# Kernel tuning notes

Measured on AMD Instinct MI355X. Metric: run time of the kernel, lower is better.

## Reference

```python
import jax, jax.numpy as jnp
import numpy as np

N_EMBD = 1024
N_HEAD = 16
HEAD_DIM = N_EMBD // N_HEAD
SCALE = 1.0 / np.sqrt(HEAD_DIM).astype(np.float32)


def setup_inputs() -> dict:
    key = jax.random.key(0)
    ks = jax.random.split(key, 9)
    B, T = 2, 2048
    std = 1.0 / np.sqrt(N_EMBD).astype(np.float32)
    x = jax.random.normal(ks[0], (B, T, N_EMBD), dtype=jnp.float32)
    Wq = jax.random.normal(ks[1], (N_EMBD, N_EMBD), dtype=jnp.float32) * std
    Wk = jax.random.normal(ks[2], (N_EMBD, N_EMBD), dtype=jnp.float32) * std
    Wv = jax.random.normal(ks[3], (N_EMBD, N_EMBD), dtype=jnp.float32) * std
    Wo = jax.random.normal(ks[4], (N_EMBD, N_EMBD), dtype=jnp.float32) * std
    bq = jax.random.normal(ks[5], (N_EMBD,), dtype=jnp.float32) * 0.01
    bk = jax.random.normal(ks[6], (N_EMBD,), dtype=jnp.float32) * 0.01
    bv = jax.random.normal(ks[7], (N_EMBD,), dtype=jnp.float32) * 0.01
    bo = jax.random.normal(ks[8], (N_EMBD,), dtype=jnp.float32) * 0.01
    return {"x": x, "Wq": Wq, "bq": bq, "Wk": Wk, "bk": bk,
            "Wv": Wv, "bv": bv, "Wo": Wo, "bo": bo}


def reference(x, Wq, bq, Wk, bk, Wv, bv, Wo, bo):
    B, T, C = x.shape
    # project and split heads: (B, H, T, D)
    def heads(y):
        return y.reshape(B, T, N_HEAD, HEAD_DIM).transpose(0, 2, 1, 3)
    q = heads(x @ Wq.T + bq)
    k = heads(x @ Wk.T + bk)
    v = heads(x @ Wv.T + bv)
    # materialized causal attention (matches the torch module's math)
    att = jnp.einsum("bhqd,bhkd->bhqk", q, k) * SCALE
    causal = jnp.tril(jnp.ones((T, T), dtype=bool))
    att = jnp.where(causal, att, -jnp.inf)
    att = jax.nn.softmax(att, axis=-1)
    out = jnp.einsum("bhqk,bhkd->bhqd", att, v)
    out = out.transpose(0, 2, 1, 3).reshape(B, T, C)
    return out @ Wo.T + bo
```

## Files before the change

kernel.cpp:

```cpp
#include <hip/hip_runtime.h>
#include <stdint.h>

typedef unsigned short u16;
typedef __attribute__((ext_vector_type(8))) short short8;
typedef __attribute__((ext_vector_type(4))) float f32x4;
typedef __attribute__((ext_vector_type(16))) float f32x16;

__device__ __forceinline__ u16 f2bf(float f) {
  union { float f; unsigned int u; } c; c.f = f;
  return (u16)((c.u + 0x7FFFu + ((c.u >> 16) & 1u)) >> 16);
}

__device__ __forceinline__ float bf2f(u16 v) {
  union { unsigned int u; float f; } c; c.u = ((unsigned int)v) << 16;
  return c.f;
}

__device__ __forceinline__ f32x4 mfma16(short8 a, short8 b, f32x4 c) {
  return __builtin_amdgcn_mfma_f32_16x16x32_bf16(a, b, c, 0, 0, 0);
}

__device__ __forceinline__ f32x16 mfma32(short8 a, short8 b, f32x16 c) {
  return __builtin_amdgcn_mfma_f32_32x32x16_bf16(a, b, c, 0, 0, 0);
}

__device__ __forceinline__ void gl_lds16(const u16* g, u16* l) {
  __builtin_amdgcn_global_load_lds((const __attribute__((address_space(1))) void*)g,
                                   (__attribute__((address_space(3))) void*)l, 16, 0, 0);
}

__global__ __launch_bounds__(256) void cast_all(
    const float* __restrict__ x, const float* __restrict__ wq, const float* __restrict__ wk,
    const float* __restrict__ wv, const float* __restrict__ wo,
    u16* __restrict__ xb, u16* __restrict__ wqb, u16* __restrict__ wkb,
    u16* __restrict__ wvb, u16* __restrict__ wob) {
  int b = blockIdx.x;
  const float* src; u16* dst; int i;
  if (b < 4096)      { src = x;  dst = xb;  i = b * 256 + threadIdx.x; }
  else if (b < 5120) { src = wq; dst = wqb; i = (b - 4096) * 256 + threadIdx.x; }
  else if (b < 6144) { src = wk; dst = wkb; i = (b - 5120) * 256 + threadIdx.x; }
  else if (b < 7168) { src = wv; dst = wvb; i = (b - 6144) * 256 + threadIdx.x; }
  else               { src = wo; dst = wob; i = (b - 7168) * 256 + threadIdx.x; }
  float4 v = ((const float4*)src)[i];
  ushort4 o;
  o.x = f2bf(v.x); o.y = f2bf(v.y); o.z = f2bf(v.z); o.w = f2bf(v.w);
  ((ushort4*)dst)[i] = o;
}

__global__ __launch_bounds__(256) void qkv_gemm(
    const u16* __restrict__ xb, const u16* __restrict__ wqb, const u16* __restrict__ wkb,
    const u16* __restrict__ wvb, const float* __restrict__ bq, const float* __restrict__ bk,
    const float* __restrict__ bv, u16* __restrict__ Qb, u16* __restrict__ Kb,
    u16* __restrict__ VTb) {
  __shared__ __align__(16) u16 As[2][128 * 64];
  __shared__ __align__(16) u16 Bs[2][128 * 64];
  const int id = blockIdx.x;
  const int s = id >> 3;
  const int mblk = (id & 7) + ((s & 3) << 3);
  const int z = (s >> 2) % 3;
  const int nblk = s / 12;
  const u16* __restrict__ W = (z == 0) ? wqb : (z == 1) ? wkb : wvb;
  const float* __restrict__ bias = (z == 0) ? bq : (z == 1) ? bk : bv;
  const int m0 = mblk * 128, n0 = nblk * 128;
  const int tid = threadIdx.x, lane = tid & 63, wave = tid >> 6;
  const int wr = (wave >> 1) * 64, wc = (wave & 1) * 64;
  const int fr = lane & 15, fg = lane >> 4;
  const int lrow = lane >> 3;
  const int lcol = (((lane & 7) ^ (lrow & 7)) * 8);

  const u16* ga = xb + (size_t)(m0 + wave * 32 + lrow) * 1024 + lcol;
  const u16* gb = W  + (size_t)(n0 + wave * 32 + lrow) * 1024 + lcol;

  auto stage = [&](int k0, int b) {
    u16* la = As[b] + wave * 2048;
    u16* lb = Bs[b] + wave * 2048;
#pragma unroll
    for (int i = 0; i < 4; ++i) {
      gl_lds16(ga + k0 + (size_t)(8 * i) * 1024, la + i * 512);
      gl_lds16(gb + k0 + (size_t)(8 * i) * 1024, lb + i * 512);
    }
  };

  f32x4 acc[4][4] = {};

  stage(0, 0);
  asm volatile("s_waitcnt vmcnt(0)" ::: "memory");
  __builtin_amdgcn_s_barrier();
  __builtin_amdgcn_sched_barrier(0);

  for (int t = 0; t < 16; ++t) {
    const int cur = t & 1;
    if (t < 15) stage((t + 1) * 64, cur ^ 1);
    __builtin_amdgcn_sched_barrier(0);
    const u16* Ac = As[cur];
    const u16* Bc = Bs[cur];
#pragma unroll
    for (int kk = 0; kk < 2; ++kk) {
      short8 a[4], b[4];
#pragma unroll
      for (int i = 0; i < 4; ++i)
        a[i] = *(const short8*)(Ac + (wr + i * 16 + fr) * 64 +
                                (((kk * 4 + fg) ^ (fr & 7)) * 8));
#pragma unroll
      for (int i = 0; i < 4; ++i)
        b[i] = *(const short8*)(Bc + (wc + i * 16 + fr) * 64 +
                                (((kk * 4 + fg) ^ (fr & 7)) * 8));
      __builtin_amdgcn_s_setprio(1);
#pragma unroll
      for (int i = 0; i < 4; ++i)
#pragma unroll
        for (int j = 0; j < 4; ++j) acc[i][j] = mfma16(a[i], b[j], acc[i][j]);
      __builtin_amdgcn_s_setprio(0);
    }
    asm volatile("s_waitcnt vmcnt(0)" ::: "memory");
    __builtin_amdgcn_s_barrier();
    __builtin_amdgcn_sched_barrier(0);
  }

  const float qsc = (z == 0) ? (0.125f * 1.44269504088896f) : 1.0f;
#pragma unroll
  for (int j = 0; j < 4; ++j) {
    const int col = n0 + wc + j * 16 + fr;
    const float bcol = bias[col];
    const int h = col >> 6, d = col & 63;
#pragma unroll
    for (int i = 0; i < 4; ++i) {
#pragma unroll
      for (int r = 0; r < 4; ++r) {
        const int m = m0 + wr + i * 16 + fg * 4 + r;
        const int bi = m >> 11, t = m & 2047;
        const u16 o = f2bf((acc[i][j][r] + bcol) * qsc);
        const size_t bse = (size_t)(bi * 16 + h) << 17;
        if (z == 0)      Qb[bse + (size_t)t * 64 + d] = o;
        else if (z == 1) Kb[bse + (size_t)t * 64 + d] = o;
        else             VTb[bse + (size_t)d * 2048 + t] = o;
      }
    }
  }
}

__global__ __launch_bounds__(256, 2) void attn_kernel(
    const u16* __restrict__ Qb, const u16* __restrict__ Kb, const u16* __restrict__ VTb,
    u16* __restrict__ aOb) {
  __shared__ __align__(16) char smem[49152];
  __shared__ float Mll[4][2][64];
  u16* Ow = (u16*)smem;
  const int id = blockIdx.x;
  const int xcd = id & 7, wbl = id >> 3;
  const int cu = wbl & 31, rr = wbl >> 5;
  const int g = cu >> 2;
  const int bh = xcd + ((cu & 3) << 3);
  const int j = (rr == 0) ? 31 - g : (rr == 1) ? 16 + g : (rr == 2) ? 15 - g : g;
  const int tid = threadIdx.x, lane = tid & 63, wave = tid >> 6;
  const int l31 = lane & 31, hi = lane >> 5;
  const size_t base = (size_t)bh << 17;
  const int bi = bh >> 4, h = bh & 15;
  const int q0 = j * 64;

  u16* kb0 = (u16*)(smem + wave * 12288);
  u16* kb1 = (u16*)(smem + wave * 12288 + 4096);
  u16* vb  = (u16*)(smem + wave * 12288 + 8192);

  short8 qf[2][4];
  {
    const u16* qp = Qb + base + (size_t)(q0 + l31) * 64 + hi * 8;
#pragma unroll
    for (int mi = 0; mi < 2; ++mi)
#pragma unroll
      for (int st = 0; st < 4; ++st)
        qf[mi][st] = *(const short8*)(qp + mi * 32 * 64 + st * 16);
  }

  f32x16 oacc[2][2] = {};
  float lrun[2] = {0.f, 0.f};

  auto stageK = [&](int t0, u16* kb) {
    const u16* kp = Kb + base + (size_t)(t0 + (lane >> 3)) * 64 +
                    (((lane & 7) ^ ((lane >> 3) & 7)) * 8);
#pragma unroll
    for (int i = 0; i < 4; ++i) gl_lds16(kp + (size_t)(8 * i) * 64, kb + i * 512);
  };
  auto stageV = [&](int t0) {
    const u16* vp = VTb + base + (size_t)(lane >> 2) * 2048 + t0 +
                    (((lane & 3) ^ ((lane >> 2) & 3)) * 8);
#pragma unroll
    for (int i = 0; i < 4; ++i) gl_lds16(vp + (size_t)(16 * i) * 2048, vb + i * 512);
  };

  const int tmax = 2 * j + 1;
  if (wave <= tmax) {
    int buf = 0;
    stageK(wave * 32, kb0);
    stageV(wave * 32);
    for (int tu = wave; tu <= tmax; tu += 4) {
      const int t0 = tu * 32;
      const bool more = (tu + 4 <= tmax);
      if (more) {
        stageK((tu + 4) * 32, buf ? kb0 : kb1);
        asm volatile("s_waitcnt vmcnt(4)" ::: "memory");
      } else {
        asm volatile("s_waitcnt vmcnt(0)" ::: "memory");
      }
      __builtin_amdgcn_sched_barrier(0);
      const char* kb = (const char*)(buf ? kb1 : kb0);

      short8 kf[4];
#pragma unroll
      for (int st = 0; st < 4; ++st)
        kf[st] = *(const short8*)(kb + l31 * 128 + (((st * 2 + hi) ^ (l31 & 7)) << 4));
      short8 vf[2][2];
#pragma unroll
      for (int nb = 0; nb < 2; ++nb)
#pragma unroll
        for (int ks = 0; ks < 2; ++ks)
          vf[nb][ks] = *(const short8*)((const char*)vb + (nb * 32 + l31) * 64 +
                                        (((ks * 2 + hi) ^ (l31 & 3)) << 4));

#pragma unroll
      for (int mi = 0; mi < 2; ++mi) {
        f32x16 s = {};
        __builtin_amdgcn_s_setprio(1);
        s = mfma32(kf[0], qf[mi][0], s);
        s = mfma32(kf[1], qf[mi][1], s);
        s = mfma32(kf[2], qf[mi][2], s);
        s = mfma32(kf[3], qf[mi][3], s);
        __builtin_amdgcn_s_setprio(0);

        if (t0 + 31 > q0 + mi * 32) {
          const int qv = q0 + mi * 32 + l31;
#pragma unroll
          for (int r = 0; r < 16; ++r) {
            const int tl = t0 + (r & 3) + ((r >> 2) << 3) + hi * 4;
            if (tl > qv) s[r] = -1e30f;
          }
        }

        float rs = 0.f;
#pragma unroll
        for (int r = 0; r < 16; ++r) {
          const float pv = exp2f(s[r]);
          s[r] = pv;
          rs += pv;
        }
        lrun[mi] += rs;

        uint32_t w0, w1, w2, w3, w4, w5, w6, w7;
        asm("v_cvt_pk_bf16_f32 %0, %1, %2" : "=v"(w0) : "v"(s[0]),  "v"(s[1]));
        asm("v_cvt_pk_bf16_f32 %0, %1, %2" : "=v"(w1) : "v"(s[2]),  "v"(s[3]));
        asm("v_cvt_pk_bf16_f32 %0, %1, %2" : "=v"(w2) : "v"(s[4]),  "v"(s[5]));
        asm("v_cvt_pk_bf16_f32 %0, %1, %2" : "=v"(w3) : "v"(s[6]),  "v"(s[7]));
        asm("v_cvt_pk_bf16_f32 %0, %1, %2" : "=v"(w4) : "v"(s[8]),  "v"(s[9]));
        asm("v_cvt_pk_bf16_f32 %0, %1, %2" : "=v"(w5) : "v"(s[10]), "v"(s[11]));
        asm("v_cvt_pk_bf16_f32 %0, %1, %2" : "=v"(w6) : "v"(s[12]), "v"(s[13]));
        asm("v_cvt_pk_bf16_f32 %0, %1, %2" : "=v"(w7) : "v"(s[14]), "v"(s[15]));
        asm("v_permlane32_swap_b32 %0, %1" : "+v"(w0), "+v"(w2));
        asm("v_permlane32_swap_b32 %0, %1" : "+v"(w1), "+v"(w3));
        asm("v_permlane32_swap_b32 %0, %1" : "+v"(w4), "+v"(w6));
        asm("v_permlane32_swap_b32 %0, %1" : "+v"(w5), "+v"(w7));
        short8 pa0, pa1;
        {
          uint32_t* p0 = (uint32_t*)&pa0;
          p0[0] = w0; p0[1] = w1; p0[2] = w2; p0[3] = w3;
          uint32_t* p1 = (uint32_t*)&pa1;
          p1[0] = w4; p1[1] = w5; p1[2] = w6; p1[3] = w7;
        }

        __builtin_amdgcn_s_setprio(1);
        oacc[mi][0] = mfma32(pa0, vf[0][0], oacc[mi][0]);
        oacc[mi][0] = mfma32(pa1, vf[0][1], oacc[mi][0]);
        oacc[mi][1] = mfma32(pa0, vf[1][0], oacc[mi][1]);
        oacc[mi][1] = mfma32(pa1, vf[1][1], oacc[mi][1]);
        __builtin_amdgcn_s_setprio(0);
      }

      if (more) {
        asm volatile("s_waitcnt lgkmcnt(0)" ::: "memory");
        __builtin_amdgcn_sched_barrier(0);
        stageV((tu + 4) * 32);
      }
      buf ^= 1;
    }
  }

  __syncthreads();
#pragma unroll
  for (int mi = 0; mi < 2; ++mi) Mll[wave][hi][mi * 32 + l31] = lrun[mi];
#pragma unroll
  for (int mi = 0; mi < 2; ++mi)
#pragma unroll
    for (int nb = 0; nb < 2; ++nb)
#pragma unroll
      for (int r = 0; r < 16; ++r) {
        const int q = mi * 32 + (r & 3) + ((r >> 2) << 3) + hi * 4;
        Ow[(wave * 64 + q) * 72 + nb * 32 + l31] = f2bf(oacc[mi][nb][r]);
      }
  __syncthreads();

  const int rq = tid >> 2, c0 = (tid & 3) * 16;
  float lt = 0.f;
#pragma unroll
  for (int w = 0; w < 4; ++w)
#pragma unroll
    for (int gg = 0; gg < 2; ++gg) lt += Mll[w][gg][rq];
  const float inv = __builtin_amdgcn_rcpf(lt);
  float o[16] = {};
#pragma unroll
  for (int w = 0; w < 4; ++w) {
    const u16* orow = &Ow[(w * 64 + rq) * 72 + c0];
    short8 a = *(const short8*)orow;
    short8 b = *(const short8*)(orow + 8);
#pragma unroll
    for (int i = 0; i < 8; ++i) {
      o[i]     += bf2f((u16)a[i]);
      o[8 + i] += bf2f((u16)b[i]);
    }
  }
  short8 r0, r1;
#pragma unroll
  for (int i = 0; i < 8; ++i) {
    r0[i] = (short)f2bf(o[i] * inv);
    r1[i] = (short)f2bf(o[8 + i] * inv);
  }
  u16* op = aOb + ((size_t)bi * 2048 + q0 + rq) * 1024 + h * 64 + c0;
  *(short8*)op = r0;
  *(short8*)(op + 8) = r1;
}

__global__ __launch_bounds__(256) void out_gemm(
    const u16* __restrict__ Ab, const u16* __restrict__ Wb, const float* __restrict__ bo,
    float* __restrict__ out) {
  __shared__ __align__(16) u16 As[2][128 * 64];
  __shared__ __align__(16) u16 Bs[2][128 * 64];
  const int id = blockIdx.x;
  const int s = id >> 3;
  const int m0 = ((id & 7) + ((s & 3) << 3)) * 128;
  const int n0 = (s >> 2) * 128;
  const int tid = threadIdx.x, lane = tid & 63, wave = tid >> 6;
  const int wr = (wave >> 1) * 64, wc = (wave & 1) * 64;
  const int fr = lane & 15, fg = lane >> 4;
  const int lrow = lane >> 3;
  const int lcol = (((lane & 7) ^ (lrow & 7)) * 8);

  const u16* ga = Ab + (size_t)(m0 + wave * 32 + lrow) * 1024 + lcol;
  const u16* gb = Wb + (size_t)(n0 + wave * 32 + lrow) * 1024 + lcol;

  auto stage = [&](int k0, int b) {
    u16* la = As[b] + wave * 2048;
    u16* lb = Bs[b] + wave * 2048;
#pragma unroll
    for (int i = 0; i < 4; ++i) {
      gl_lds16(ga + k0 + (size_t)(8 * i) * 1024, la + i * 512);
      gl_lds16(gb + k0 + (size_t)(8 * i) * 1024, lb + i * 512);
    }
  };

  f32x4 acc[4][4] = {};

  stage(0, 0);
  asm volatile("s_waitcnt vmcnt(0)" ::: "memory");
  __builtin_amdgcn_s_barrier();
  __builtin_amdgcn_sched_barrier(0);

  for (int t = 0; t < 16; ++t) {
    const int cur = t & 1;
    if (t < 15) stage((t + 1) * 64, cur ^ 1);
    __builtin_amdgcn_sched_barrier(0);
    const u16* Ac = As[cur];
    const u16* Bc = Bs[cur];
#pragma unroll
    for (int kk = 0; kk < 2; ++kk) {
      short8 a[4], b[4];
#pragma unroll
      for (int i = 0; i < 4; ++i)
        a[i] = *(const short8*)(Ac + (wr + i * 16 + fr) * 64 +
                                (((kk * 4 + fg) ^ (fr & 7)) * 8));
#pragma unroll
      for (int i = 0; i < 4; ++i)
        b[i] = *(const short8*)(Bc + (wc + i * 16 + fr) * 64 +
                                (((kk * 4 + fg) ^ (fr & 7)) * 8));
      __builtin_amdgcn_s_setprio(1);
#pragma unroll
      for (int i = 0; i < 4; ++i)
#pragma unroll
        for (int j = 0; j < 4; ++j) acc[i][j] = mfma16(a[i], b[j], acc[i][j]);
      __builtin_amdgcn_s_setprio(0);
    }
    asm volatile("s_waitcnt vmcnt(0)" ::: "memory");
    __builtin_amdgcn_s_barrier();
    __builtin_amdgcn_sched_barrier(0);
  }

#pragma unroll
  for (int j = 0; j < 4; ++j) {
    const int col = n0 + wc + j * 16 + fr;
    const float bcol = bo[col];
#pragma unroll
    for (int i = 0; i < 4; ++i)
#pragma unroll
      for (int r = 0; r < 4; ++r) {
        const int m = m0 + wr + i * 16 + fg * 4 + r;
        out[(size_t)m * 1024 + col] = acc[i][j][r] + bcol;
      }
  }
}

extern "C" void kernel_launch(void* const* d_in, const int* in_sizes, int n_in,
                              void* d_out, int out_size, void* d_ws, size_t ws_size,
                              hipStream_t stream) {
  (void)in_sizes; (void)n_in; (void)out_size; (void)ws_size;
  const float* x  = (const float*)d_in[0];
  const float* Wq = (const float*)d_in[1];
  const float* bq = (const float*)d_in[2];
  const float* Wk = (const float*)d_in[3];
  const float* bk = (const float*)d_in[4];
  const float* Wv = (const float*)d_in[5];
  const float* bv = (const float*)d_in[6];
  const float* Wo = (const float*)d_in[7];
  const float* bo = (const float*)d_in[8];
  float* out = (float*)d_out;
  char* ws = (char*)d_ws;

  const size_t MB = 1024 * 1024;
  u16* xb  = (u16*)(ws);
  u16* wqb = (u16*)(ws + 8 * MB);
  u16* wkb = (u16*)(ws + 10 * MB);
  u16* wvb = (u16*)(ws + 12 * MB);
  u16* wob = (u16*)(ws + 14 * MB);
  u16* Qb  = (u16*)(ws + 16 * MB);
  u16* Kb  = (u16*)(ws + 24 * MB);
  u16* VTb = (u16*)(ws + 32 * MB);
  u16* aOb = (u16*)(ws + 40 * MB);

  cast_all<<<8192, 256, 0, stream>>>(x, Wq, Wk, Wv, Wo, xb, wqb, wkb, wvb, wob);
  qkv_gemm<<<768, 256, 0, stream>>>(xb, wqb, wkb, wvb, bq, bk, bv, Qb, Kb, VTb);
  attn_kernel<<<1024, 256, 0, stream>>>(Qb, Kb, VTb, aOb);
  out_gemm<<<256, 256, 0, stream>>>(aOb, wob, bo, out);
}
```

Measured before the change: 123.8 us.

## Give each wave private LDS tiles in QKV and output GEMMs, dropping block barriers

Each wave now loads only its own 64x32 slices of A and B into a private LDS region, so the per-iteration block-wide s_barrier and full vmcnt(0) waits are gone. The loop uses a K-step of 32 with a partial vmcnt wait, so the next stage's loads stay in flight while the current one is consumed. QKV block indexing is also changed so the projection index z is the outermost dimension. The cost is no sharing of A/B tiles between waves: each wave fetches its own copy, doubling global/L2 traffic per block. The loop also runs twice as many iterations, each with less work.

```diff
diff --git a/kernel.cpp b/kernel.cpp
--- a/kernel.cpp
+++ b/kernel.cpp
@@ -52,68 +52,67 @@
     const u16* __restrict__ wvb, const float* __restrict__ bq, const float* __restrict__ bk,
     const float* __restrict__ bv, u16* __restrict__ Qb, u16* __restrict__ Kb,
     u16* __restrict__ VTb) {
-  __shared__ __align__(16) u16 As[2][128 * 64];
-  __shared__ __align__(16) u16 Bs[2][128 * 64];
+  __shared__ __align__(16) char smem[65536];
   const int id = blockIdx.x;
-  const int s = id >> 3;
-  const int mblk = (id & 7) + ((s & 3) << 3);
-  const int z = (s >> 2) % 3;
-  const int nblk = s / 12;
+  const int z = id >> 8;
+  const int u = id & 255;
+  const int mblk = (u & 7) + (((u >> 3) & 3) << 3);
+  const int nblk = u >> 5;
   const u16* __restrict__ W = (z == 0) ? wqb : (z == 1) ? wkb : wvb;
   const float* __restrict__ bias = (z == 0) ? bq : (z == 1) ? bk : bv;
   const int m0 = mblk * 128, n0 = nblk * 128;
   const int tid = threadIdx.x, lane = tid & 63, wave = tid >> 6;
   const int wr = (wave >> 1) * 64, wc = (wave & 1) * 64;
   const int fr = lane & 15, fg = lane >> 4;
-  const int lrow = lane >> 3;
-  const int lcol = (((lane & 7) ^ (lrow & 7)) * 8);
-
-  const u16* ga = xb + (size_t)(m0 + wave * 32 + lrow) * 1024 + lcol;
-  const u16* gb = W  + (size_t)(n0 + wave * 32 + lrow) * 1024 + lcol;
+  const int r16 = lane >> 2;
+  const int cswz = (lane & 3) ^ (r16 & 3);
+
+  u16* la0 = (u16*)(smem + wave * 16384);
+  u16* la1 = (u16*)(smem + wave * 16384 + 4096);
+  u16* lb0 = (u16*)(smem + wave * 16384 + 8192);
+  u16* lb1 = (u16*)(smem + wave * 16384 + 12288);
+
+  const u16* gA = xb + (size_t)(m0 + wr + r16) * 1024 + cswz * 8;
+  const u16* gB = W  + (size_t)(n0 + wc + r16) * 1024 + cswz * 8;
 
   auto stage = [&](int k0, int b) {
-    u16* la = As[b] + wave * 2048;
-    u16* lb = Bs[b] + wave * 2048;
+    u16* la = b ? la1 : la0;
+    u16* lb = b ? lb1 : lb0;
 #pragma unroll
     for (int i = 0; i < 4; ++i) {
-      gl_lds16(ga + k0 + (size_t)(8 * i) * 1024, la + i * 512);
-      gl_lds16(gb + k0 + (size_t)(8 * i) * 1024, lb + i * 512);
+      gl_lds16(gA + k0 + (size_t)(i * 16) * 1024, la + i * 512);
+      gl_lds16(gB + k0 + (size_t)(i * 16) * 1024, lb + i * 512);
     }
   };
 
   f32x4 acc[4][4] = {};
-
   stage(0, 0);
-  asm volatile("s_waitcnt vmcnt(0)" ::: "memory");
-  __builtin_amdgcn_s_barrier();
-  __builtin_amdgcn_sched_barrier(0);
-
-  for (int t = 0; t < 16; ++t) {
+
+  for (int t = 0; t < 32; ++t) {
     const int cur = t & 1;
-    if (t < 15) stage((t + 1) * 64, cur ^ 1);
+    if (t < 31) {
+      stage((t + 1) * 32, cur ^ 1);
+      asm volatile("s_waitcnt vmcnt(8)" ::: "memory");
+    } else {
+      asm volatile("s_waitcnt vmcnt(0)" ::: "memory");
+    }
     __builtin_amdgcn_sched_barrier(0);
-    const u16* Ac = As[cur];
-    const u16* Bc = Bs[cur];
-#pragma unroll
-    for (int kk = 0; kk < 2; ++kk) {
-      short8 a[4], b[4];
-#pragma unroll
-      for (int i = 0; i < 4; ++i)
-        a[i] = *(const short8*)(Ac + (wr + i * 16 + fr) * 64 +
-                                (((kk * 4 + fg) ^ (fr & 7)) * 8));
-#pragma unroll
-      for (int i = 0; i < 4; ++i)
-        b[i] = *(const short8*)(Bc + (wc + i * 16 + fr) * 64 +
-                                (((kk * 4 + fg) ^ (fr & 7)) * 8));
-      __builtin_amdgcn_s_setprio(1);
-#pragma unroll
-      for (int i = 0; i < 4; ++i)
-#pragma unroll
-        for (int j = 0; j < 4; ++j) acc[i][j] = mfma16(a[i], b[j], acc[i][j]);
-      __builtin_amdgcn_s_setprio(0);
-    }
-    asm volatile("s_waitcnt vmcnt(0)" ::: "memory");
-    __builtin_amdgcn_s_barrier();
+    const u16* Ac = cur ? la1 : la0;
+    const u16* Bc = cur ? lb1 : lb0;
+    short8 a[4], b[4];
+#pragma unroll
+    for (int i = 0; i < 4; ++i)
+      a[i] = *(const short8*)(Ac + (i * 16 + fr) * 32 + ((fg ^ (fr & 3)) * 8));
+#pragma unroll
+    for (int i = 0; i < 4; ++i)
+      b[i] = *(const short8*)(Bc + (i * 16 + fr) * 32 + ((fg ^ (fr & 3)) * 8));
+    __builtin_amdgcn_s_setprio(1);
+#pragma unroll
+    for (int i = 0; i < 4; ++i)
+#pragma unroll
+      for (int j = 0; j < 4; ++j) acc[i][j] = mfma16(a[i], b[j], acc[i][j]);
+    __builtin_amdgcn_s_setprio(0);
+    asm volatile("s_waitcnt lgkmcnt(0)" ::: "memory");
     __builtin_amdgcn_sched_barrier(0);
   }
 
@@ -329,8 +328,7 @@
 __global__ __launch_bounds__(256) void out_gemm(
     const u16* __restrict__ Ab, const u16* __restrict__ Wb, const float* __restrict__ bo,
     float* __restrict__ out) {
-  __shared__ __align__(16) u16 As[2][128 * 64];
-  __shared__ __align__(16) u16 Bs[2][128 * 64];
+  __shared__ __align__(16) char smem[65536];
   const int id = blockIdx.x;
   const int s = id >> 3;
   const int m0 = ((id & 7) + ((s & 3) << 3)) * 128;
@@ -338,55 +336,55 @@
   const int tid = threadIdx.x, lane = tid & 63, wave = tid >> 6;
   const int wr = (wave >> 1) * 64, wc = (wave & 1) * 64;
   const int fr = lane & 15, fg = lane >> 4;
-  const int lrow = lane >> 3;
-  const int lcol = (((lane & 7) ^ (lrow & 7)) * 8);
-
-  const u16* ga = Ab + (size_t)(m0 + wave * 32 + lrow) * 1024 + lcol;
-  const u16* gb = Wb + (size_t)(n0 + wave * 32 + lrow) * 1024 + lcol;
+  const int r16 = lane >> 2;
+  const int cswz = (lane & 3) ^ (r16 & 3);
+
+  u16* la0 = (u16*)(smem + wave * 16384);
+  u16* la1 = (u16*)(smem + wave * 16384 + 4096);
+  u16* lb0 = (u16*)(smem + wave * 16384 + 8192);
+  u16* lb1 = (u16*)(smem + wave * 16384 + 12288);
+
+  const u16* gA = Ab + (size_t)(m0 + wr + r16) * 1024 + cswz * 8;
+  const u16* gB = Wb + (size_t)(n0 + wc + r16) * 1024 + cswz * 8;
 
   auto stage = [&](int k0, int b) {
-    u16* la = As[b] + wave * 2048;
-    u16* lb = Bs[b] + wave * 2048;
+    u16* la = b ? la1 : la0;
+    u16* lb = b ? lb1 : lb0;
 #pragma unroll
     for (int i = 0; i < 4; ++i) {
-      gl_lds16(ga + k0 + (size_t)(8 * i) * 1024, la + i * 512);
-      gl_lds16(gb + k0 + (size_t)(8 * i) * 1024, lb + i * 512);
+      gl_lds16(gA + k0 + (size_t)(i * 16) * 1024, la + i * 512);
+      gl_lds16(gB + k0 + (size_t)(i * 16) * 1024, lb + i * 512);
     }
   };
 
   f32x4 acc[4][4] = {};
-
   stage(0, 0);
-  asm volatile("s_waitcnt vmcnt(0)" ::: "memory");
-  __builtin_amdgcn_s_barrier();
-  __builtin_amdgcn_sched_barrier(0);
-
-  for (int t = 0; t < 16; ++t) {
+
+  for (int t = 0; t < 32; ++t) {
     const int cur = t & 1;
-    if (t < 15) stage((t + 1) * 64, cur ^ 1);
+    if (t < 31) {
+      stage((t + 1) * 32, cur ^ 1);
+      asm volatile("s_waitcnt vmcnt(8)" ::: "memory");
+    } else {
+      asm volatile("s_waitcnt vmcnt(0)" ::: "memory");
+    }
     __builtin_amdgcn_sched_barrier(0);
-    const u16* Ac = As[cur];
-    const u16* Bc = Bs[cur];
-#pragma unroll
-    for (int kk = 0; kk < 2; ++kk) {
-      short8 a[4], b[4];
-#pragma unroll
-      for (int i = 0; i < 4; ++i)
-        a[i] = *(const short8*)(Ac + (wr + i * 16 + fr) * 64 +
-                                (((kk * 4 + fg) ^ (fr & 7)) * 8));
-#pragma unroll
-      for (int i = 0; i < 4; ++i)
-        b[i] = *(const short8*)(Bc + (wc + i * 16 + fr) * 64 +
-                                (((kk * 4 + fg) ^ (fr & 7)) * 8));
-      __builtin_amdgcn_s_setprio(1);
-#pragma unroll
-      for (int i = 0; i < 4; ++i)
-#pragma unroll
-        for (int j = 0; j < 4; ++j) acc[i][j] = mfma16(a[i], b[j], acc[i][j]);
-      __builtin_amdgcn_s_setprio(0);
-    }
-    asm volatile("s_waitcnt vmcnt(0)" ::: "memory");
-    __builtin_amdgcn_s_barrier();
+    const u16* Ac = cur ? la1 : la0;
+    const u16* Bc = cur ? lb1 : lb0;
+    short8 a[4], b[4];
+#pragma unroll
+    for (int i = 0; i < 4; ++i)
+      a[i] = *(const short8*)(Ac + (i * 16 + fr) * 32 + ((fg ^ (fr & 3)) * 8));
+#pragma unroll
+    for (int i = 0; i < 4; ++i)
+      b[i] = *(const short8*)(Bc + (i * 16 + fr) * 32 + ((fg ^ (fr & 3)) * 8));
+    __builtin_amdgcn_s_setprio(1);
+#pragma unroll
+    for (int i = 0; i < 4; ++i)
+#pragma unroll
+      for (int j = 0; j < 4; ++j) acc[i][j] = mfma16(a[i], b[j], acc[i][j]);
+    __builtin_amdgcn_s_setprio(0);
+    asm volatile("s_waitcnt lgkmcnt(0)" ::: "memory");
     __builtin_amdgcn_sched_barrier(0);
   }
 
```

After: 118.8 us. 4.0% less time.
